# Performance work log

Measured on AMD Instinct MI355X. Metric: run time of the kernel, lower is better.

The kernel has to match this reference:

```python
import jax, jax.numpy as jnp
import numpy as np

D_MODEL = 384
D_INNER = 768          # 2 * d_model (mamba expand=2)
DT_RANK = 24           # ceil(d_model / 16)
D_STATE = 16
DEPTH = 24
KCONV = 4
BATCH = 2
FRAMES = 8
GRID = 14              # 224 / 16
NTOK = GRID * GRID     # 196 spatial tokens
PS = 16                # patch size
EPS = 1e-5


def setup_inputs() -> dict:
    key = jax.random.key(0)
    ks = iter(jax.random.split(key, 32))
    r = lambda shape, s=0.02: jax.random.normal(next(ks), shape, jnp.float32) * s
    A_init = jnp.tile(jnp.log(jnp.arange(1, D_STATE + 1, dtype=jnp.float32)),
                      (DEPTH, D_INNER, 1))
    return {
        "x": jax.random.normal(next(ks), (BATCH, 3, FRAMES, PS * GRID, PS * GRID), jnp.float32),
        "patch_w": r((D_MODEL, 3 * PS * PS)),
        "patch_b": jnp.zeros((D_MODEL,), jnp.float32),
        "pos_embed": r((NTOK, D_MODEL)),
        "temp_pos": r((FRAMES, D_MODEL)),
        "in_proj": r((DEPTH, 2 * D_INNER, D_MODEL)),
        "conv_w": r((DEPTH, D_INNER, KCONV), 0.2),
        "conv_b": jnp.zeros((DEPTH, D_INNER), jnp.float32),
        "xproj_w": r((DEPTH, DT_RANK + 2 * D_STATE, D_INNER)),
        "dt_w": r((DEPTH, D_INNER, DT_RANK), 0.1),
        "dt_b": jnp.full((DEPTH, D_INNER), -2.0, jnp.float32),
        "A_log": A_init,
        "Dp": jnp.ones((DEPTH, D_INNER), jnp.float32),
        "conv_w_bwd": r((DEPTH, D_INNER, KCONV), 0.2),
        "conv_b_bwd": jnp.zeros((DEPTH, D_INNER), jnp.float32),
        "xproj_w_bwd": r((DEPTH, DT_RANK + 2 * D_STATE, D_INNER)),
        "dt_w_bwd": r((DEPTH, D_INNER, DT_RANK), 0.1),
        "dt_b_bwd": jnp.full((DEPTH, D_INNER), -2.0, jnp.float32),
        "A_log_bwd": A_init,
        "Dp_bwd": jnp.ones((DEPTH, D_INNER), jnp.float32),
        "out_proj": r((DEPTH, D_MODEL, D_INNER)),
        "norm_w": jnp.ones((DEPTH, D_MODEL), jnp.float32),
        "norm_f": jnp.ones((D_MODEL,), jnp.float32),
    }


def _rmsnorm(x, w):
    x32 = x.astype(jnp.float32)
    return x32 * jax.lax.rsqrt(jnp.mean(x32 * x32, axis=-1, keepdims=True) + EPS) * w


def _causal_conv(x, w, b):
    # x: [B, d_inner, L], depthwise causal conv, kernel KCONV
    xp = jnp.pad(x, ((0, 0), (0, 0), (KCONV - 1, 0)))
    y = jax.lax.conv_general_dilated(
        xp, w[:, None, :], window_strides=(1,), padding="VALID",
        dimension_numbers=("NCH", "OIH", "NCH"), feature_group_count=D_INNER)
    return y + b[None, :, None]


def _ssm_branch(x, z, conv_w, conv_b, xproj, dtw, dtb, A_log, Dp):
    # x, z: [B, d_inner, L]
    xc = jax.nn.silu(_causal_conv(x, conv_w, conv_b))
    xdbl = jnp.einsum("bdl,kd->bkl", xc, xproj)          # [B, dt_rank+2n, L]
    dt = jax.nn.softplus(
        jnp.einsum("brl,dr->bdl", xdbl[:, :DT_RANK], dtw) + dtb[None, :, None])
    Bm = xdbl[:, DT_RANK:DT_RANK + D_STATE]               # [B, n, L]
    Cm = xdbl[:, DT_RANK + D_STATE:]                      # [B, n, L]
    A = -jnp.exp(A_log)                                   # [d, n]
    dA = jnp.exp(jnp.einsum("bdl,dn->lbdn", dt, A))      # [L, B, d, n]
    dBu = jnp.einsum("bdl,bnl->lbdn", dt * xc, Bm)       # [L, B, d, n]
    Cl = jnp.moveaxis(Cm, -1, 0)                          # [L, B, n]

    def step(h, inp):
        a, bu, c = inp
        h = a * h + bu
        return h, jnp.einsum("bdn,bn->bd", h, c)

    h0 = jnp.zeros((x.shape[0], D_INNER, D_STATE), x.dtype)
    _, ys = jax.lax.scan(step, h0, (dA, dBu, Cl))         # ys: [L, B, d]
    y = jnp.moveaxis(ys, 0, -1) + Dp[None, :, None] * xc  # [B, d, L]
    return y * jax.nn.silu(z)


def reference(x, patch_w, patch_b, pos_embed, temp_pos, in_proj,
              conv_w, conv_b, xproj_w, dt_w, dt_b, A_log, Dp,
              conv_w_bwd, conv_b_bwd, xproj_w_bwd, dt_w_bwd, dt_b_bwd,
              A_log_bwd, Dp_bwd, out_proj, norm_w, norm_f):
    B, _, T, _, _ = x.shape
    # PatchEmbed: Conv3d with kernel=stride=(1,16,16) == per-patch matmul
    xt = x.transpose(0, 2, 1, 3, 4).reshape(B * T, 3, GRID, PS, GRID, PS)
    patches = xt.transpose(0, 2, 4, 1, 3, 5).reshape(B * T, NTOK, 3 * PS * PS)
    tok = patches @ patch_w.T + patch_b                   # [B*T, N, D]
    tok = tok + pos_embed[None]
    tok = tok.reshape(B, T, NTOK, D_MODEL) + temp_pos[None, :, None, :]
    hidden = tok.reshape(B, T * NTOK, D_MODEL)            # [B, L, D]
    residual = jnp.zeros_like(hidden)

    params = (in_proj, conv_w, conv_b, xproj_w, dt_w, dt_b, A_log, Dp,
              conv_w_bwd, conv_b_bwd, xproj_w_bwd, dt_w_bwd, dt_b_bwd,
              A_log_bwd, Dp_bwd, out_proj, norm_w)

    def block(carry, p):
        (ipw, cw, cb, xpw, dw, db, al, dp,
         cw_b, cb_b, xpw_b, dw_b, db_b, al_b, dp_b, opw, nw) = p
        h, res = carry
        res = res + h                                     # fused add (fp32 residual)
        h = _rmsnorm(res, nw)
        xz = jnp.einsum("bld,ed->bel", h, ipw)            # [B, 2*d_inner, L]
        xi, zi = xz[:, :D_INNER], xz[:, D_INNER:]
        yf = _ssm_branch(xi, zi, cw, cb, xpw, dw, db, al, dp)
        yb = jnp.flip(_ssm_branch(jnp.flip(xi, -1), jnp.flip(zi, -1),
                                  cw_b, cb_b, xpw_b, dw_b, db_b, al_b, dp_b), -1)
        out = jnp.einsum("bdl,od->blo", yf + yb, opw)     # out_proj
        return (out, res), None

    (hidden, residual), _ = jax.lax.scan(block, (hidden, residual), params)
    # final fused add + RMSNorm
    return _rmsnorm(residual + hidden, norm_f)            # [B, T*N, D]
```

## Files before the change

### kernel.cpp

```cpp
#include <hip/hip_runtime.h>
#include <hip/hip_bf16.h>

typedef unsigned short ushort_t;
typedef short bf16x8 __attribute__((ext_vector_type(8)));
typedef unsigned short us16x8 __attribute__((ext_vector_type(8)));
typedef float f32x4  __attribute__((ext_vector_type(4)));

#define BATCH   2
#define FRAMES  8
#define GRID_   14
#define NTOK    196
#define PS      16
#define IMG     224
#define L_SEQ   1568
#define DM      384
#define DI      768
#define DTR     24
#define DS      16
#define DEPTH   24
#define KCONV   4
#define NROWS   (BATCH*L_SEQ)
#define EPS_    1e-5f
#define NCHUNK  32
#define CLEN    49
#define DTILE   64
#define NDC     (DI/DTILE)
#define LOG2E   1.4426950408889634f

__device__ __forceinline__ ushort_t f2us(float f){
    __hip_bfloat16 h = __float2bfloat16(f);
    return *reinterpret_cast<ushort_t*>(&h);
}
__device__ __forceinline__ float us2f(ushort_t u){
    return __uint_as_float(((unsigned int)u) << 16);
}
__device__ __forceinline__ ushort4 f4tous4(float4 v){
    ushort4 o;
    o.x = f2us(v.x); o.y = f2us(v.y); o.z = f2us(v.z); o.w = f2us(v.w);
    return o;
}

__global__ __launch_bounds__(256) void patchify_kernel(const float* __restrict__ x,
                                                       ushort_t* __restrict__ patches){
    int idx4 = blockIdx.x*256 + threadIdx.x;
    if (idx4 >= NROWS*768/4) return;
    int idx = idx4*4;
    int k   = idx % 768;
    int r   = idx / 768;
    int tok = r % NTOK;
    int bt  = r / NTOK;
    int t = bt % FRAMES, b = bt / FRAMES;
    int gy = tok / GRID_, gx = tok % GRID_;
    int c = k / 256; int rem = k % 256; int py = rem/16, px = rem%16;
    long xo = (((long)(b*3 + c)*FRAMES + t)*IMG + (gy*PS+py))*IMG + (gx*PS+px);
    float4 v = *(const float4*)(x + xo);
    *(ushort4*)(patches + idx) = f4tous4(v);
}

__global__ __launch_bounds__(256) void convert_kernel(const float* __restrict__ in,
                                                      ushort_t* __restrict__ out, int n){
    int i = blockIdx.x*256 + threadIdx.x;
    if (i < n) out[i] = f2us(in[i]);
}

#define WI_SZ  (2*DI*DM)
#define WO_SZ  (DM*DI)
#define WX_SZ  (56*DI)
#define WDT_SZ (DI*32)
#define WCVT_TOTAL (WI_SZ + WO_SZ + 2*WX_SZ + 2*WDT_SZ)
#define WCVT_Q  (WCVT_TOTAL/4)

__global__ __launch_bounds__(256) void convert_group_kernel(
        const float* __restrict__ wi, const float* __restrict__ wo,
        const float* __restrict__ wxf, const float* __restrict__ wxb,
        const float* __restrict__ wdtf, const float* __restrict__ wdtb,
        ushort_t* __restrict__ out, int l0, int count)
{
    long gid = (long)blockIdx.x*256 + threadIdx.x;
    if (gid >= (long)count*WCVT_Q) return;
    int ly = (int)(gid / WCVT_Q);
    int r  = (int)(gid % WCVT_Q)*4;
    int l  = l0 + ly;
    float4 v;
    if (r < WI_SZ)                       v = *(const float4*)(wi + (long)l*WI_SZ + r);
    else if (r < WI_SZ+WO_SZ)            v = *(const float4*)(wo + (long)l*WO_SZ + r - WI_SZ);
    else if (r < WI_SZ+WO_SZ+WX_SZ)      v = *(const float4*)(wxf + (long)l*WX_SZ + r - WI_SZ - WO_SZ);
    else if (r < WI_SZ+WO_SZ+2*WX_SZ)    v = *(const float4*)(wxb + (long)l*WX_SZ + r - WI_SZ - WO_SZ - WX_SZ);
    else if (r < WI_SZ+WO_SZ+2*WX_SZ+WDT_SZ){
        int i = r - (WI_SZ+WO_SZ+2*WX_SZ);
        int rr = i >> 5, c = i & 31;
        v = (c < DTR) ? *(const float4*)(wdtf + (long)l*DI*DTR + rr*DTR + c)
                      : float4{0.f,0.f,0.f,0.f};
    } else {
        int i = r - (WI_SZ+WO_SZ+2*WX_SZ+WDT_SZ);
        int rr = i >> 5, c = i & 31;
        v = (c < DTR) ? *(const float4*)(wdtb + (long)l*DI*DTR + rr*DTR + c)
                      : float4{0.f,0.f,0.f,0.f};
    }
    *(ushort4*)(out + (long)ly*WCVT_TOTAL + r) = f4tous4(v);
}

template<int MT, int STAGE>
__global__ __launch_bounds__(256) void gemm_mfma_kernel(
        const ushort_t* __restrict__ A, int lda, long strideA,
        const ushort_t* __restrict__ W, int ldw, long strideW,
        int K, int N,
        float* __restrict__ out0, long strideO0,
        ushort_t* __restrict__ outb0, ushort_t* __restrict__ outb1, long strideOb,
        int mode,
        const float* __restrict__ aux0, const float* __restrict__ aux1,
        const float* __restrict__ aux2)
{
    int z = blockIdx.z;
    A += (long)z * strideA;
    W += (long)z * strideW;
    if (out0)  out0  += (long)z * strideO0;
    if (outb0) outb0 += (long)z * strideOb;

    int tid  = threadIdx.x;
    int wave = tid >> 6, lane = tid & 63;
    int l15 = lane & 15, quad = lane >> 4;
    int m0 = blockIdx.y * (MT*16), n0 = blockIdx.x * 64;

    const ushort_t* wp = W + (long)(n0 + wave*16 + l15)*ldw + quad*8;

    f32x4 acc[MT];
    #pragma unroll
    for (int mt = 0; mt < MT; mt++) acc[mt] = f32x4{0,0,0,0};

    if constexpr (STAGE){
        __shared__ alignas(16) ushort_t As[2][MT*16][40];
        bool act = (tid < MT*64);
        int srow = tid >> 2, skq = tid & 3;
        const ushort_t* ag = A + (long)(m0 + srow)*lda + skq*8;
        us16x8 av = {};
        if (act) av = *(const us16x8*)ag;
        int nIter = K >> 5;
        for (int it = 0; it < nIter; it++){
            if (act) *(us16x8*)&As[it&1][srow][skq*8] = av;
            if (act && it+1 < nIter) av = *(const us16x8*)(ag + (long)(it+1)*32);
            __syncthreads();
            bf16x8 bfrag = *reinterpret_cast<const bf16x8*>(wp + it*32);
            #pragma unroll
            for (int mt = 0; mt < MT; mt++){
                bf16x8 afrag = *reinterpret_cast<const bf16x8*>(&As[it&1][mt*16+l15][quad*8]);
                acc[mt] = __builtin_amdgcn_mfma_f32_16x16x32_bf16(afrag, bfrag, acc[mt], 0, 0, 0);
            }
        }
    } else {
        const ushort_t* ap0 = A + (long)(m0 + l15)*lda + quad*8;
        for (int k0 = 0; k0 < K; k0 += 32){
            bf16x8 bfrag = *reinterpret_cast<const bf16x8*>(wp + k0);
            #pragma unroll
            for (int mt = 0; mt < MT; mt++){
                bf16x8 afrag = *reinterpret_cast<const bf16x8*>(ap0 + (long)mt*16*lda + k0);
                acc[mt] = __builtin_amdgcn_mfma_f32_16x16x32_bf16(afrag, bfrag, acc[mt], 0, 0, 0);
            }
        }
    }

    int cn = n0 + wave*16 + l15;
    #pragma unroll
    for (int mt = 0; mt < MT; mt++){
        #pragma unroll
        for (int r = 0; r < 4; r++){
            int row = m0 + mt*16 + quad*4 + r;
            float v = acc[mt][r];
            if (mode == 0){
                out0[(long)row*N + cn] += v;
            } else if (mode == 1){
                if (cn < DI) outb0[(long)row*DI + cn] = f2us(v);
                else         outb1[(long)row*DI + cn - DI] = f2us(v);
            } else if (mode == 2){
                int tok = row % NTOK, t = (row/NTOK) % FRAMES;
                out0[(long)row*N + cn] = v + aux0[cn] + aux1[tok*DM+cn] + aux2[t*DM+cn];
            } else if (mode == 3){
                const float* bias = z ? aux1 : aux0;
                float xs = v + bias[cn];
                float sp = (xs > 20.f) ? xs : log1pf(__expf(xs));
                outb0[(long)row*N + cn] = f2us(sp);
            } else {
                if (cn < 56) out0[(long)row*56 + cn] = v;
                if (cn < 32) outb0[(long)row*32 + cn] = f2us(cn < DTR ? v : 0.f);
            }
        }
    }
}

__global__ __launch_bounds__(128) void rmsnorm_kernel(
        const float* __restrict__ res,
        ushort_t* __restrict__ outb, const float* __restrict__ w)
{
    int r = blockIdx.x; int tid = threadIdx.x;
    const float* rr = res + (long)r*DM;
    float v[3]; float ss = 0.f;
    #pragma unroll
    for (int i = 0; i < 3; i++){
        int c = tid + i*128;
        float x = rr[c];
        v[i] = x; ss += x*x;
    }
    #pragma unroll
    for (int off = 32; off; off >>= 1) ss += __shfl_down(ss, off, 64);
    __shared__ float wsum[2];
    if ((tid & 63) == 0) wsum[tid >> 6] = ss;
    __syncthreads();
    float scale = rsqrtf((wsum[0] + wsum[1]) / (float)DM + EPS_);
    #pragma unroll
    for (int i = 0; i < 3; i++){
        int c = tid + i*128;
        outb[(long)r*DM + c] = f2us(v[i] * scale * w[c]);
    }
}

__global__ __launch_bounds__(256) void conv_kernel(
        const ushort_t* __restrict__ xi,
        const float* __restrict__ cw_f, const float* __restrict__ cb_f,
        const float* __restrict__ cw_b, const float* __restrict__ cb_b,
        ushort_t* __restrict__ xcb)
{
    int vidx = blockIdx.x*256 + threadIdx.x;
    if (vidx >= 2*NROWS*192) return;
    int dq = vidx % 192; int d4 = dq*4;
    int r2 = vidx / 192;
    int dir = r2 / NROWS;
    int rr  = r2 % NROWS;
    int b = rr / L_SEQ, p = rr % L_SEQ;
    const float* cw = dir ? cw_b : cw_f;
    const float* cb = dir ? cb_b : cb_f;
    float w[4][4];
    #pragma unroll
    for (int dd = 0; dd < 4; dd++){
        float4 wv = *(const float4*)(cw + (d4+dd)*KCONV);
        w[dd][0]=wv.x; w[dd][1]=wv.y; w[dd][2]=wv.z; w[dd][3]=wv.w;
    }
    float4 acc = *(const float4*)(cb + d4);
    #pragma unroll
    for (int j = 0; j < KCONV; j++){
        int pp = p - (KCONV-1) + j;
        if (pp >= 0){
            int phys = dir ? (L_SEQ-1-pp) : pp;
            ushort4 u = *(const ushort4*)(xi + ((long)b*L_SEQ + phys)*DI + d4);
            acc.x += w[0][j]*us2f(u.x);
            acc.y += w[1][j]*us2f(u.y);
            acc.z += w[2][j]*us2f(u.z);
            acc.w += w[3][j]*us2f(u.w);
        }
    }
    ushort4 ob;
    ob.x = f2us(acc.x/(1.f+__expf(-acc.x)));
    ob.y = f2us(acc.y/(1.f+__expf(-acc.y)));
    ob.z = f2us(acc.z/(1.f+__expf(-acc.z)));
    ob.w = f2us(acc.w/(1.f+__expf(-acc.w)));
    *(ushort4*)(xcb + (long)r2*DI + d4) = ob;
}

__global__ __launch_bounds__(256) void scan_pass1_kernel(
        const ushort_t* __restrict__ xcb, const ushort_t* __restrict__ dtb,
        const float* __restrict__ xdbl2,
        const float* __restrict__ Alog_f, const float* __restrict__ Alog_b,
        float* __restrict__ Pbuf, float* __restrict__ Sbuf)
{
    int dchunk = blockIdx.x;
    int chunk  = blockIdx.y;
    int z      = blockIdx.z;
    int b = z & 1, dir = z >> 1;
    int tid = threadIdx.x;
    int dl = tid >> 2, nq = tid & 3;
    int dbase = dchunk*DTILE;
    int d = dbase + dl;

    const ushort_t* xc = xcb + (long)dir*NROWS*DI;
    const ushort_t* dt = dtb + (long)dir*NROWS*DI;
    const float* xd = xdbl2 + (long)dir*NROWS*56;
    const float* Alog = dir ? Alog_b : Alog_f;

    float Av2[4];
    #pragma unroll
    for (int j = 0; j < 4; j++)
        Av2[j] = -__expf(Alog[d*DS + nq*4 + j]) * LOG2E;

    __shared__ ushort_t sdt[CLEN][DTILE], sxc[CLEN][DTILE];
    __shared__ float sB[CLEN][16];
    int c0 = chunk * CLEN;
    for (int e = tid; e < CLEN*16; e += 256){
        int s = e >> 4, q4 = (e & 15)*4;
        long row = (long)b*L_SEQ + c0 + s;
        *(ushort4*)&sdt[s][q4] = *(const ushort4*)(dt + row*DI + dbase + q4);
        *(ushort4*)&sxc[s][q4] = *(const ushort4*)(xc + row*DI + dbase + q4);
    }
    for (int e = tid; e < CLEN*4; e += 256){
        int s = e >> 2, q4 = (e & 3)*4;
        long row = (long)b*L_SEQ + c0 + s;
        *(float4*)&sB[s][q4] = *(const float4*)(xd + row*56 + DTR + q4);
    }
    __syncthreads();

    float h0=0.f,h1=0.f,h2=0.f,h3=0.f, dts=0.f;
    for (int s = 0; s < CLEN; s++){
        float dtv = us2f(sdt[s][dl]), xcv = us2f(sxc[s][dl]);
        float4 Bv = *(float4*)&sB[s][nq*4];
        float tmp = dtv*xcv;
        dts += dtv;
        h0 = exp2f(dtv*Av2[0])*h0 + tmp*Bv.x;
        h1 = exp2f(dtv*Av2[1])*h1 + tmp*Bv.y;
        h2 = exp2f(dtv*Av2[2])*h2 + tmp*Bv.z;
        h3 = exp2f(dtv*Av2[3])*h3 + tmp*Bv.w;
    }
    long idx = (((long)z*NCHUNK + chunk)*DI + d)*DS + nq*4;
    float4 P; P.x=exp2f(Av2[0]*dts); P.y=exp2f(Av2[1]*dts);
    P.z=exp2f(Av2[2]*dts); P.w=exp2f(Av2[3]*dts);
    float4 S; S.x=h0; S.y=h1; S.z=h2; S.w=h3;
    *(float4*)(Pbuf + idx) = P;
    *(float4*)(Sbuf + idx) = S;
}

__global__ __launch_bounds__(256) void scan_combine_kernel(
        const float* __restrict__ Pbuf, float* __restrict__ Sbuf)
{
    int gid = blockIdx.x*256 + threadIdx.x;
    if (gid >= 4*DI*DS/4) return;
    int dn4 = (gid % (DI*DS/4))*4;
    int z   = gid / (DI*DS/4);
    long idx = (long)z*NCHUNK*DI*DS + dn4;
    float4 hin = {0.f,0.f,0.f,0.f};
    for (int cg = 0; cg < NCHUNK; cg += 8){
        float4 P[8], S[8];
        #pragma unroll
        for (int j = 0; j < 8; j++){
            P[j] = *(const float4*)(Pbuf + idx + (long)j*DI*DS);
            S[j] = *(const float4*)(Sbuf + idx + (long)j*DI*DS);
        }
        #pragma unroll
        for (int j = 0; j < 8; j++){
            *(float4*)(Sbuf + idx + (long)j*DI*DS) = hin;
            hin.x = P[j].x*hin.x + S[j].x;
            hin.y = P[j].y*hin.y + S[j].y;
            hin.z = P[j].z*hin.z + S[j].z;
            hin.w = P[j].w*hin.w + S[j].w;
        }
        idx += (long)8*DI*DS;
    }
}

__global__ __launch_bounds__(256) void scan_pass2_kernel(
        const ushort_t* __restrict__ xcb, const ushort_t* __restrict__ dtb,
        const float* __restrict__ xdbl2,
        const float* __restrict__ Alog_f, const float* __restrict__ Dp_f,
        const float* __restrict__ Alog_b, const float* __restrict__ Dp_b,
        const float* __restrict__ Hbuf,
        ushort_t* __restrict__ ys_f, ushort_t* __restrict__ ys_b)
{
    int dchunk = blockIdx.x;
    int chunk  = blockIdx.y;
    int z      = blockIdx.z;
    int b = z & 1, dir = z >> 1;
    int tid = threadIdx.x;
    int dl = tid >> 2, nq = tid & 3;
    int dbase = dchunk*DTILE;
    int d = dbase + dl;

    const ushort_t* xc = xcb + (long)dir*NROWS*DI;
    const ushort_t* dt = dtb + (long)dir*NROWS*DI;
    const float* xd = xdbl2 + (long)dir*NROWS*56;
    const float* Alog = dir ? Alog_b : Alog_f;
    const float* Dpp  = dir ? Dp_b   : Dp_f;
    ushort_t* ys = dir ? ys_b : ys_f;

    float Av2[4];
    #pragma unroll
    for (int j = 0; j < 4; j++)
        Av2[j] = -__expf(Alog[d*DS + nq*4 + j]) * LOG2E;
    float Dval = Dpp[d];

    __shared__ ushort_t sdt[CLEN][DTILE], sxc[CLEN][DTILE], sy[CLEN][DTILE];
    __shared__ float sB[CLEN][16], sC[CLEN][16];
    int c0 = chunk * CLEN;
    for (int e = tid; e < CLEN*16; e += 256){
        int s = e >> 4, q4 = (e & 15)*4;
        long row = (long)b*L_SEQ + c0 + s;
        *(ushort4*)&sdt[s][q4] = *(const ushort4*)(dt + row*DI + dbase + q4);
        *(ushort4*)&sxc[s][q4] = *(const ushort4*)(xc + row*DI + dbase + q4);
    }
    for (int e = tid; e < CLEN*4; e += 256){
        int s = e >> 2, q4 = (e & 3)*4;
        long row = (long)b*L_SEQ + c0 + s;
        *(float4*)&sB[s][q4] = *(const float4*)(xd + row*56 + DTR + q4);
        *(float4*)&sC[s][q4] = *(const float4*)(xd + row*56 + DTR + DS + q4);
    }
    __syncthreads();

    long idx = (((long)z*NCHUNK + chunk)*DI + d)*DS + nq*4;
    float4 H = *(const float4*)(Hbuf + idx);
    float h0=H.x, h1=H.y, h2=H.z, h3=H.w;

    for (int s = 0; s < CLEN; s++){
        float dtv = us2f(sdt[s][dl]), xcv = us2f(sxc[s][dl]);
        float4 Bv = *(float4*)&sB[s][nq*4];
        float4 Cv = *(float4*)&sC[s][nq*4];
        float tmp = dtv*xcv;
        h0 = exp2f(dtv*Av2[0])*h0 + tmp*Bv.x;
        h1 = exp2f(dtv*Av2[1])*h1 + tmp*Bv.y;
        h2 = exp2f(dtv*Av2[2])*h2 + tmp*Bv.z;
        h3 = exp2f(dtv*Av2[3])*h3 + tmp*Bv.w;
        float c = h0*Cv.x + h1*Cv.y + h2*Cv.z + h3*Cv.w;
        c += __shfl_xor(c, 1);
        c += __shfl_xor(c, 2);
        if (nq == 0) sy[s][dl] = f2us(c + Dval*xcv);
    }
    __syncthreads();

    for (int e = tid; e < CLEN*16; e += 256){
        int s = e >> 4, q4 = (e & 15)*4;
        int p = c0 + s;
        int phys = dir ? (L_SEQ-1-p) : p;
        *(ushort4*)(ys + ((long)b*L_SEQ + phys)*DI + dbase + q4) = *(ushort4*)&sy[s][q4];
    }
}

__global__ __launch_bounds__(256) void ys_gate_kernel(
        const ushort_t* __restrict__ ysf, const ushort_t* __restrict__ ysb,
        const ushort_t* __restrict__ zi, ushort_t* __restrict__ out)
{
    int i4 = (blockIdx.x*256 + threadIdx.x)*4;
    if (i4 >= NROWS*DI) return;
    ushort4 a = *(const ushort4*)(ysf + i4);
    ushort4 bb = *(const ushort4*)(ysb + i4);
    ushort4 u = *(const ushort4*)(zi + i4);
    ushort4 r;
    {
        float zv = us2f(u.x); float g = zv/(1.f+__expf(-zv));
        r.x = f2us((us2f(a.x)+us2f(bb.x))*g);
    }{
        float zv = us2f(u.y); float g = zv/(1.f+__expf(-zv));
        r.y = f2us((us2f(a.y)+us2f(bb.y))*g);
    }{
        float zv = us2f(u.z); float g = zv/(1.f+__expf(-zv));
        r.z = f2us((us2f(a.z)+us2f(bb.z))*g);
    }{
        float zv = us2f(u.w); float g = zv/(1.f+__expf(-zv));
        r.w = f2us((us2f(a.w)+us2f(bb.w))*g);
    }
    *(ushort4*)(out + i4) = r;
}

__global__ __launch_bounds__(128) void rmsnorm_final_kernel(
        const float* __restrict__ res,
        const float* __restrict__ w, float* __restrict__ out)
{
    int r = blockIdx.x; int tid = threadIdx.x;
    const float* rr = res + (long)r*DM;
    float v[3]; float ss = 0.f;
    #pragma unroll
    for (int i = 0; i < 3; i++){
        int c = tid + i*128;
        float x = rr[c];
        v[i] = x; ss += x*x;
    }
    #pragma unroll
    for (int off = 32; off; off >>= 1) ss += __shfl_down(ss, off, 64);
    __shared__ float wsum[2];
    if ((tid & 63) == 0) wsum[tid >> 6] = ss;
    __syncthreads();
    float scale = rsqrtf((wsum[0] + wsum[1]) / (float)DM + EPS_);
    #pragma unroll
    for (int i = 0; i < 3; i++){
        int c = tid + i*128;
        out[(long)r*DM + c] = v[i] * scale * w[c];
    }
}

extern "C" void kernel_launch(void* const* d_in, const int* in_sizes, int n_in,
                              void* d_out, int out_size, void* d_ws, size_t ws_size,
                              hipStream_t stream)
{
    const float* x         = (const float*)d_in[0];
    const float* patch_w   = (const float*)d_in[1];
    const float* patch_b   = (const float*)d_in[2];
    const float* pos_embed = (const float*)d_in[3];
    const float* temp_pos  = (const float*)d_in[4];
    const float* in_proj   = (const float*)d_in[5];
    const float* conv_w    = (const float*)d_in[6];
    const float* conv_b    = (const float*)d_in[7];
    const float* xproj_w   = (const float*)d_in[8];
    const float* dt_w      = (const float*)d_in[9];
    const float* dt_b      = (const float*)d_in[10];
    const float* A_log     = (const float*)d_in[11];
    const float* Dp        = (const float*)d_in[12];
    const float* conv_w_b  = (const float*)d_in[13];
    const float* conv_b_b  = (const float*)d_in[14];
    const float* xproj_w_b = (const float*)d_in[15];
    const float* dt_w_b    = (const float*)d_in[16];
    const float* dt_b_b    = (const float*)d_in[17];
    const float* A_log_b   = (const float*)d_in[18];
    const float* Dp_b      = (const float*)d_in[19];
    const float* out_proj  = (const float*)d_in[20];
    const float* norm_w    = (const float*)d_in[21];
    const float* norm_f    = (const float*)d_in[22];

    float* ws = (float*)d_ws;
    size_t off = 0;
    float* residual = ws + off; off += (size_t)NROWS*DM;
    float* hnormreg = ws + off; off += (size_t)NROWS*DM/2;
    float* xireg    = ws + off; off += (size_t)NROWS*DI/2;
    float* zireg    = ws + off; off += (size_t)NROWS*DI/2;
    float* xc2bfreg = ws + off; off += (size_t)NROWS*DI;
    float* xdbl2    = ws + off; off += (size_t)2*NROWS*56;
    float* xdblbf_f = ws + off; off += (size_t)2*NROWS*32/2;
    float* dt2bfreg = ws + off; off += (size_t)NROWS*DI;
    float* ysfbfreg = ws + off; off += (size_t)NROWS*DI/2;
    float* ysbbfreg = ws + off; off += (size_t)NROWS*DI/2;
    float* Sbuf     = ws + off; off += (size_t)4*NCHUNK*DI*DS;
    float* wpbf_f   = ws + off; off += (size_t)(DM*DI+1)/2;
    size_t fixed_floats = off;
    const size_t perW = (size_t)(WCVT_TOTAL+1)/2;
    int G = (ws_size/4 >= fixed_floats + 24*perW) ? 24
          : (ws_size/4 >= fixed_floats + 8*perW)  ? 8 : 1;
    float* wbf_f = ws + off; off += G*perW;

    ushort_t* hnorm_bf   = (ushort_t*)hnormreg;
    ushort_t* xi_bf      = (ushort_t*)xireg;
    ushort_t* zi_bf      = (ushort_t*)zireg;
    ushort_t* ys_bf      = (ushort_t*)zireg;
    ushort_t* xc2_bf     = (ushort_t*)xc2bfreg;
    ushort_t* xdbl_bf    = (ushort_t*)xdblbf_f;
    ushort_t* dt2_bf     = (ushort_t*)dt2bfreg;
    ushort_t* ysf_bf     = (ushort_t*)ysfbfreg;
    ushort_t* ysb_bf     = (ushort_t*)ysbbfreg;
    ushort_t* patches_bf = (ushort_t*)dt2bfreg;
    ushort_t* wbuf       = (ushort_t*)wbf_f;
    ushort_t* wp_bf      = (ushort_t*)wpbf_f;
    float* Pbuf = hnormreg;

    patchify_kernel<<<(NROWS*768/4+255)/256, 256, 0, stream>>>(x, patches_bf);
    convert_kernel<<<(DM*DI+255)/256, 256, 0, stream>>>(patch_w, wp_bf, DM*DI);
    gemm_mfma_kernel<4,1><<<dim3(DM/64, NROWS/64, 1), 256, 0, stream>>>(
        patches_bf, DI, 0, wp_bf, DI, 0, DI, DM,
        residual, 0, nullptr, nullptr, 0, 2, patch_b, pos_embed, temp_pos);

    for (int l = 0; l < DEPTH; l++){
        if (l % G == 0){
            int cnt = (DEPTH - l < G) ? DEPTH - l : G;
            long total = (long)cnt*WCVT_Q;
            convert_group_kernel<<<(int)((total+255)/256), 256, 0, stream>>>(
                in_proj, out_proj, xproj_w, xproj_w_b, dt_w, dt_w_b,
                wbuf, l, cnt);
        }
        ushort_t* wl = wbuf + (size_t)(l % G)*WCVT_TOTAL;
        ushort_t* wi_bf  = wl;
        ushort_t* wo_bf  = wl + WI_SZ;
        ushort_t* wx_bf  = wl + WI_SZ + WO_SZ;
        ushort_t* wdt_bf = wl + WI_SZ + WO_SZ + 2*WX_SZ;

        rmsnorm_kernel<<<NROWS, 128, 0, stream>>>(residual, hnorm_bf,
                                                  norm_w + (size_t)l*DM);
        gemm_mfma_kernel<4,1><<<dim3(2*DI/64, NROWS/64, 1), 256, 0, stream>>>(
            hnorm_bf, DM, 0, wi_bf, DM, 0, DM, 2*DI,
            nullptr, 0, xi_bf, zi_bf, 0, 1, nullptr, nullptr, nullptr);

        conv_kernel<<<(2*NROWS*192+255)/256, 256, 0, stream>>>(
            xi_bf, conv_w + (size_t)l*DI*KCONV, conv_b + (size_t)l*DI,
            conv_w_b + (size_t)l*DI*KCONV, conv_b_b + (size_t)l*DI, xc2_bf);

        gemm_mfma_kernel<1,1><<<dim3(1, NROWS/16, 2), 256, 0, stream>>>(
            xc2_bf, DI, (long)NROWS*DI, wx_bf, DI, WX_SZ, DI, 64,
            xdbl2, (long)NROWS*56, xdbl_bf, nullptr, (long)NROWS*32, 4,
            nullptr, nullptr, nullptr);

        gemm_mfma_kernel<4,0><<<dim3(DI/64, NROWS/64, 2), 256, 0, stream>>>(
            xdbl_bf, 32, (long)NROWS*32, wdt_bf, 32, WDT_SZ, 32, DI,
            nullptr, 0, dt2_bf, nullptr, (long)NROWS*DI, 3,
            dt_b + (size_t)l*DI, dt_b_b + (size_t)l*DI, nullptr);

        scan_pass1_kernel<<<dim3(NDC, NCHUNK, 4), 256, 0, stream>>>(
            xc2_bf, dt2_bf, xdbl2, A_log + (size_t)l*DI*DS, A_log_b + (size_t)l*DI*DS,
            Pbuf, Sbuf);
        scan_combine_kernel<<<(4*DI*DS/4+255)/256, 256, 0, stream>>>(Pbuf, Sbuf);
        scan_pass2_kernel<<<dim3(NDC, NCHUNK, 4), 256, 0, stream>>>(
            xc2_bf, dt2_bf, xdbl2,
            A_log + (size_t)l*DI*DS, Dp + (size_t)l*DI,
            A_log_b + (size_t)l*DI*DS, Dp_b + (size_t)l*DI,
            Sbuf, ysf_bf, ysb_bf);

        ys_gate_kernel<<<(NROWS*DI/4+255)/256, 256, 0, stream>>>(ysf_bf, ysb_bf, zi_bf, ys_bf);

        gemm_mfma_kernel<4,1><<<dim3(DM/64, NROWS/64, 1), 256, 0, stream>>>(
            ys_bf, DI, 0, wo_bf, DI, 0, DI, DM,
            residual, 0, nullptr, nullptr, 0, 0, nullptr, nullptr, nullptr);
    }

    rmsnorm_final_kernel<<<NROWS, 128, 0, stream>>>(residual, norm_f, (float*)d_out);
}
```

Before: 4.188 ms.

## Fuse forward/backward scan pass2 with SiLU gating into one kernel

Each pass2 block now runs both the forward chunk and its mirrored backward chunk for the same batch and channel tile. It sums the two outputs in fp32 shared memory and applies the SiLU(z) gate before writing the gated bf16 result straight to ys. This removes the separate ys_gate kernel launch and the round trip of the ys_f/ys_b intermediates through global memory. In exchange the grid shrinks by half and each block runs two sequential scans, so there is less parallelism and a longer critical path per block, and it uses more shared memory.

```diff
diff --git a/kernel.cpp b/kernel.cpp
--- a/kernel.cpp
+++ b/kernel.cpp
@@ -349,99 +349,111 @@
         const float* __restrict__ Alog_f, const float* __restrict__ Dp_f,
         const float* __restrict__ Alog_b, const float* __restrict__ Dp_b,
         const float* __restrict__ Hbuf,
-        ushort_t* __restrict__ ys_f, ushort_t* __restrict__ ys_b)
+        const ushort_t* __restrict__ zi,
+        ushort_t* __restrict__ ys)
 {
     int dchunk = blockIdx.x;
-    int chunk  = blockIdx.y;
-    int z      = blockIdx.z;
-    int b = z & 1, dir = z >> 1;
+    int chunkf = blockIdx.y;
+    int b      = blockIdx.z;
     int tid = threadIdx.x;
     int dl = tid >> 2, nq = tid & 3;
     int dbase = dchunk*DTILE;
     int d = dbase + dl;
-
-    const ushort_t* xc = xcb + (long)dir*NROWS*DI;
-    const ushort_t* dt = dtb + (long)dir*NROWS*DI;
-    const float* xd = xdbl2 + (long)dir*NROWS*56;
-    const float* Alog = dir ? Alog_b : Alog_f;
-    const float* Dpp  = dir ? Dp_b   : Dp_f;
-    ushort_t* ys = dir ? ys_b : ys_f;
-
-    float Av2[4];
-    #pragma unroll
-    for (int j = 0; j < 4; j++)
-        Av2[j] = -__expf(Alog[d*DS + nq*4 + j]) * LOG2E;
-    float Dval = Dpp[d];
-
-    __shared__ ushort_t sdt[CLEN][DTILE], sxc[CLEN][DTILE], sy[CLEN][DTILE];
-    __shared__ float sB[CLEN][16], sC[CLEN][16];
-    int c0 = chunk * CLEN;
+    int chunkb = NCHUNK-1-chunkf;
+    int c0f = chunkf*CLEN, c0b = chunkb*CLEN;
+
+    float Avf[4], Avb[4];
+    #pragma unroll
+    for (int j = 0; j < 4; j++){
+        Avf[j] = -__expf(Alog_f[d*DS + nq*4 + j]) * LOG2E;
+        Avb[j] = -__expf(Alog_b[d*DS + nq*4 + j]) * LOG2E;
+    }
+    float Dvf = Dp_f[d], Dvb = Dp_b[d];
+
+    __shared__ ushort_t sdt[2][CLEN][DTILE], sxc[2][CLEN][DTILE];
+    __shared__ float sB[2][CLEN][16], sC[2][CLEN][16];
+    __shared__ float sy[CLEN][DTILE];
+
+    for (int e = tid; e < 2*CLEN*16; e += 256){
+        int dir = (e >= CLEN*16) ? 1 : 0;
+        int e2 = e - dir*CLEN*16;
+        int s = e2 >> 4, q4 = (e2 & 15)*4;
+        int c0 = dir ? c0b : c0f;
+        long row = (long)b*L_SEQ + c0 + s;
+        const ushort_t* dt = dtb + (long)dir*NROWS*DI;
+        const ushort_t* xc = xcb + (long)dir*NROWS*DI;
+        *(ushort4*)&sdt[dir][s][q4] = *(const ushort4*)(dt + row*DI + dbase + q4);
+        *(ushort4*)&sxc[dir][s][q4] = *(const ushort4*)(xc + row*DI + dbase + q4);
+    }
+    for (int e = tid; e < 2*CLEN*4; e += 256){
+        int dir = (e >= CLEN*4) ? 1 : 0;
+        int e2 = e - dir*CLEN*4;
+        int s = e2 >> 2, q4 = (e2 & 3)*4;
+        int c0 = dir ? c0b : c0f;
+        long row = (long)b*L_SEQ + c0 + s;
+        const float* xd = xdbl2 + (long)dir*NROWS*56;
+        *(float4*)&sB[dir][s][q4] = *(const float4*)(xd + row*56 + DTR + q4);
+        *(float4*)&sC[dir][s][q4] = *(const float4*)(xd + row*56 + DTR + DS + q4);
+    }
+    __syncthreads();
+
+    {
+        long idx = (((long)b*NCHUNK + chunkf)*DI + d)*DS + nq*4;
+        float4 H = *(const float4*)(Hbuf + idx);
+        float h0=H.x, h1=H.y, h2=H.z, h3=H.w;
+        for (int s = 0; s < CLEN; s++){
+            float dtv = us2f(sdt[0][s][dl]), xcv = us2f(sxc[0][s][dl]);
+            float4 Bv = *(float4*)&sB[0][s][nq*4];
+            float4 Cv = *(float4*)&sC[0][s][nq*4];
+            float tmp = dtv*xcv;
+            h0 = exp2f(dtv*Avf[0])*h0 + tmp*Bv.x;
+            h1 = exp2f(dtv*Avf[1])*h1 + tmp*Bv.y;
+            h2 = exp2f(dtv*Avf[2])*h2 + tmp*Bv.z;
+            h3 = exp2f(dtv*Avf[3])*h3 + tmp*Bv.w;
+            float c = h0*Cv.x + h1*Cv.y + h2*Cv.z + h3*Cv.w;
+            c += __shfl_xor(c, 1);
+            c += __shfl_xor(c, 2);
+            if (nq == 0) sy[s][dl] = c + Dvf*xcv;
+        }
+    }
+    {
+        long idx = (((long)(2+b)*NCHUNK + chunkb)*DI + d)*DS + nq*4;
+        float4 H = *(const float4*)(Hbuf + idx);
+        float h0=H.x, h1=H.y, h2=H.z, h3=H.w;
+        for (int s = 0; s < CLEN; s++){
+            float dtv = us2f(sdt[1][s][dl]), xcv = us2f(sxc[1][s][dl]);
+            float4 Bv = *(float4*)&sB[1][s][nq*4];
+            float4 Cv = *(float4*)&sC[1][s][nq*4];
+            float tmp = dtv*xcv;
+            h0 = exp2f(dtv*Avb[0])*h0 + tmp*Bv.x;
+            h1 = exp2f(dtv*Avb[1])*h1 + tmp*Bv.y;
+            h2 = exp2f(dtv*Avb[2])*h2 + tmp*Bv.z;
+            h3 = exp2f(dtv*Avb[3])*h3 + tmp*Bv.w;
+            float c = h0*Cv.x + h1*Cv.y + h2*Cv.z + h3*Cv.w;
+            c += __shfl_xor(c, 1);
+            c += __shfl_xor(c, 2);
+            if (nq == 0) sy[CLEN-1-s][dl] += c + Dvb*xcv;
+        }
+    }
+    __syncthreads();
+
     for (int e = tid; e < CLEN*16; e += 256){
         int s = e >> 4, q4 = (e & 15)*4;
-        long row = (long)b*L_SEQ + c0 + s;
-        *(ushort4*)&sdt[s][q4] = *(const ushort4*)(dt + row*DI + dbase + q4);
-        *(ushort4*)&sxc[s][q4] = *(const ushort4*)(xc + row*DI + dbase + q4);
-    }
-    for (int e = tid; e < CLEN*4; e += 256){
-        int s = e >> 2, q4 = (e & 3)*4;
-        long row = (long)b*L_SEQ + c0 + s;
-        *(float4*)&sB[s][q4] = *(const float4*)(xd + row*56 + DTR + q4);
-        *(float4*)&sC[s][q4] = *(const float4*)(xd + row*56 + DTR + DS + q4);
-    }
-    __syncthreads();
-
-    long idx = (((long)z*NCHUNK + chunk)*DI + d)*DS + nq*4;
-    float4 H = *(const float4*)(Hbuf + idx);
-    float h0=H.x, h1=H.y, h2=H.z, h3=H.w;
-
-    for (int s = 0; s < CLEN; s++){
-        float dtv = us2f(sdt[s][dl]), xcv = us2f(sxc[s][dl]);
-        float4 Bv = *(float4*)&sB[s][nq*4];
-        float4 Cv = *(float4*)&sC[s][nq*4];
-        float tmp = dtv*xcv;
-        h0 = exp2f(dtv*Av2[0])*h0 + tmp*Bv.x;
-        h1 = exp2f(dtv*Av2[1])*h1 + tmp*Bv.y;
-        h2 = exp2f(dtv*Av2[2])*h2 + tmp*Bv.z;
-        h3 = exp2f(dtv*Av2[3])*h3 + tmp*Bv.w;
-        float c = h0*Cv.x + h1*Cv.y + h2*Cv.z + h3*Cv.w;
-        c += __shfl_xor(c, 1);
-        c += __shfl_xor(c, 2);
-        if (nq == 0) sy[s][dl] = f2us(c + Dval*xcv);
-    }
-    __syncthreads();
-
-    for (int e = tid; e < CLEN*16; e += 256){
-        int s = e >> 4, q4 = (e & 15)*4;
-        int p = c0 + s;
-        int phys = dir ? (L_SEQ-1-p) : p;
-        *(ushort4*)(ys + ((long)b*L_SEQ + phys)*DI + dbase + q4) = *(ushort4*)&sy[s][q4];
-    }
-}
-
-__global__ __launch_bounds__(256) void ys_gate_kernel(
-        const ushort_t* __restrict__ ysf, const ushort_t* __restrict__ ysb,
-        const ushort_t* __restrict__ zi, ushort_t* __restrict__ out)
-{
-    int i4 = (blockIdx.x*256 + threadIdx.x)*4;
-    if (i4 >= NROWS*DI) return;
-    ushort4 a = *(const ushort4*)(ysf + i4);
-    ushort4 bb = *(const ushort4*)(ysb + i4);
-    ushort4 u = *(const ushort4*)(zi + i4);
-    ushort4 r;
-    {
-        float zv = us2f(u.x); float g = zv/(1.f+__expf(-zv));
-        r.x = f2us((us2f(a.x)+us2f(bb.x))*g);
-    }{
-        float zv = us2f(u.y); float g = zv/(1.f+__expf(-zv));
-        r.y = f2us((us2f(a.y)+us2f(bb.y))*g);
-    }{
-        float zv = us2f(u.z); float g = zv/(1.f+__expf(-zv));
-        r.z = f2us((us2f(a.z)+us2f(bb.z))*g);
-    }{
-        float zv = us2f(u.w); float g = zv/(1.f+__expf(-zv));
-        r.w = f2us((us2f(a.w)+us2f(bb.w))*g);
-    }
-    *(ushort4*)(out + i4) = r;
+        long prow = (long)b*L_SEQ + c0f + s;
+        ushort4 zv = *(const ushort4*)(zi + prow*DI + dbase + q4);
+        float4 yv = *(float4*)&sy[s][q4];
+        ushort4 o;
+        {
+            float z0 = us2f(zv.x); o.x = f2us(yv.x * z0/(1.f+__expf(-z0)));
+        }{
+            float z1 = us2f(zv.y); o.y = f2us(yv.y * z1/(1.f+__expf(-z1)));
+        }{
+            float z2 = us2f(zv.z); o.z = f2us(yv.z * z2/(1.f+__expf(-z2)));
+        }{
+            float z3 = us2f(zv.w); o.w = f2us(yv.w * z3/(1.f+__expf(-z3)));
+        }
+        *(ushort4*)(ys + prow*DI + dbase + q4) = o;
+    }
 }
 
 __global__ __launch_bounds__(128) void rmsnorm_final_kernel(
@@ -525,12 +537,11 @@
     ushort_t* xc2_bf     = (ushort_t*)xc2bfreg;
     ushort_t* xdbl_bf    = (ushort_t*)xdblbf_f;
     ushort_t* dt2_bf     = (ushort_t*)dt2bfreg;
-    ushort_t* ysf_bf     = (ushort_t*)ysfbfreg;
-    ushort_t* ysb_bf     = (ushort_t*)ysbbfreg;
     ushort_t* patches_bf = (ushort_t*)dt2bfreg;
     ushort_t* wbuf       = (ushort_t*)wbf_f;
     ushort_t* wp_bf      = (ushort_t*)wpbf_f;
     float* Pbuf = hnormreg;
+    (void)ysfbfreg; (void)ysbbfreg;
 
     patchify_kernel<<<(NROWS*768/4+255)/256, 256, 0, stream>>>(x, patches_bf);
     convert_kernel<<<(DM*DI+255)/256, 256, 0, stream>>>(patch_w, wp_bf, DM*DI);
@@ -576,13 +587,11 @@
             xc2_bf, dt2_bf, xdbl2, A_log + (size_t)l*DI*DS, A_log_b + (size_t)l*DI*DS,
             Pbuf, Sbuf);
         scan_combine_kernel<<<(4*DI*DS/4+255)/256, 256, 0, stream>>>(Pbuf, Sbuf);
-        scan_pass2_kernel<<<dim3(NDC, NCHUNK, 4), 256, 0, stream>>>(
+        scan_pass2_kernel<<<dim3(NDC, NCHUNK, BATCH), 256, 0, stream>>>(
             xc2_bf, dt2_bf, xdbl2,
             A_log + (size_t)l*DI*DS, Dp + (size_t)l*DI,
             A_log_b + (size_t)l*DI*DS, Dp_b + (size_t)l*DI,
-            Sbuf, ysf_bf, ysb_bf);
-
-        ys_gate_kernel<<<(NROWS*DI/4+255)/256, 256, 0, stream>>>(ysf_bf, ysb_bf, zi_bf, ys_bf);
+            Sbuf, zi_bf, ys_bf);
 
         gemm_mfma_kernel<4,1><<<dim3(DM/64, NROWS/64, 1), 256, 0, stream>>>(
             ys_bf, DI, 0, wo_bf, DI, 0, DI, DM,
```

Result: no change. 4.214 ms (+0.6%).
